# Kernel optimization log

Hardware: AMD Instinct MI355X
Metric: run time of the kernel (lower is better)

Reference implementation:

```python
import jax, jax.numpy as jnp
import numpy as np

THRESHOLD = 1.0
DECAY = 0.9


def setup_inputs() -> dict:
    key = jax.random.key(0)
    ks = jax.random.split(key, 5)
    B, T, I, H, O = 64, 256, 2048, 4096, 1024
    return {
        "x": jax.random.normal(ks[0], (B, T, I), dtype=jnp.float32),
        "W_in": jax.random.normal(ks[1], (I, H), dtype=jnp.float32) * (1.0 / np.sqrt(I)),
        "b_in": jax.random.normal(ks[2], (H,), dtype=jnp.float32) * 0.01,
        "W_out": jax.random.normal(ks[3], (H, O), dtype=jnp.float32) * (1.0 / np.sqrt(H)),
        "b_out": jax.random.normal(ks[4], (O,), dtype=jnp.float32) * 0.01,
        "m0": jnp.zeros((H,), dtype=jnp.float32),
    }


def reference(x, W_in, b_in, W_out, b_out, m0):
    # Batched input projection for all timesteps at once, then batch-mean
    # current per step: currents[t] = mean_b(Linear(x[:, t, :])).
    currents = jnp.einsum("bti,ih->th", x, W_in) / x.shape[0] + b_in  # [T, H]

    def step(m, c):
        m = DECAY * m + c                      # leaky integrate
        fired = m > THRESHOLD                  # threshold
        spike = fired.astype(m.dtype)
        m = jnp.where(fired, 0.0, m)           # reset fired neurons
        return m, spike

    _, spikes = jax.lax.scan(step, m0, currents)  # spikes: [T, H]
    agg = spikes.mean(axis=0)                     # [H]
    return agg @ W_out + b_out                    # [O]
```

## Files before the change

### kernel.cpp

```cpp
#include <hip/hip_runtime.h>

constexpr int B = 64, T = 256, I = 2048, H = 4096, O = 1024;

#define DECAY 0.9f
#define THRESH 1.0f

__global__ __launch_bounds__(256) void batch_reduce(const float* __restrict__ x,
                                                    float* __restrict__ xbar) {
    const int idx = blockIdx.x * 256 + threadIdx.x;
    const float4* x4 = (const float4*)x;
    const int stride4 = (T * I) / 4;
    float4 acc = {0.f, 0.f, 0.f, 0.f};
#pragma unroll 16
    for (int b = 0; b < B; ++b) {
        float4 v = x4[idx + b * stride4];
        acc.x += v.x; acc.y += v.y; acc.z += v.z; acc.w += v.w;
    }
    const float s = 1.0f / (float)B;
    acc.x *= s; acc.y *= s; acc.z *= s; acc.w *= s;
    ((float4*)xbar)[idx] = acc;
}

__global__ __launch_bounds__(256) void cur_init(const float* __restrict__ b_in,
                                                float* __restrict__ cur) {
    const int idx = blockIdx.x * 256 + threadIdx.x;
    const int h4 = idx & (H / 4 - 1);
    ((float4*)cur)[idx] = ((const float4*)b_in)[h4];
}

#define BM 64
#define BN 64
#define BK 16
#define KSPLIT 4
#define LDS_PAD 4

__global__ __launch_bounds__(256) void gemm_in(const float* __restrict__ A,
                                               const float* __restrict__ Bw,
                                               float* __restrict__ C) {
    __shared__ float As[BK][BM + LDS_PAD];
    __shared__ float Bs[BK][BN + LDS_PAD];

    const int tid = threadIdx.x;
    const int blockRow = blockIdx.y * BM;
    const int blockCol = blockIdx.x * BN;
    const int kBeg = blockIdx.z * (I / KSPLIT);
    const int kEnd = kBeg + (I / KSPLIT);

    const int tr = tid >> 4;
    const int tc = tid & 15;

    const int aRow = tid >> 2;
    const int aCol = (tid & 3) << 2;
    const int bRow = tid >> 4;
    const int bCol = (tid & 15) << 2;

    float acc[4][4];
#pragma unroll
    for (int i = 0; i < 4; ++i)
#pragma unroll
        for (int j = 0; j < 4; ++j) acc[i][j] = 0.f;

    for (int k0 = kBeg; k0 < kEnd; k0 += BK) {
        float4 av = *(const float4*)(&A[(blockRow + aRow) * I + k0 + aCol]);
        float4 bv = *(const float4*)(&Bw[(size_t)(k0 + bRow) * H + blockCol + bCol]);
        __syncthreads();
        As[aCol + 0][aRow] = av.x;
        As[aCol + 1][aRow] = av.y;
        As[aCol + 2][aRow] = av.z;
        As[aCol + 3][aRow] = av.w;
        *(float4*)(&Bs[bRow][bCol]) = bv;
        __syncthreads();

#pragma unroll
        for (int k = 0; k < BK; ++k) {
            float4 a = *(const float4*)(&As[k][tr << 2]);
            float4 b = *(const float4*)(&Bs[k][tc << 2]);
            const float ar[4] = {a.x, a.y, a.z, a.w};
            const float br[4] = {b.x, b.y, b.z, b.w};
#pragma unroll
            for (int i = 0; i < 4; ++i)
#pragma unroll
                for (int j = 0; j < 4; ++j) acc[i][j] += ar[i] * br[j];
        }
    }

#pragma unroll
    for (int i = 0; i < 4; ++i) {
        const int row = blockRow + (tr << 2) + i;
#pragma unroll
        for (int j = 0; j < 4; ++j) {
            atomicAdd(&C[(size_t)row * H + blockCol + (tc << 2) + j], acc[i][j]);
        }
    }
}

__global__ __launch_bounds__(256) void lif_scan(const float* __restrict__ cur,
                                                const float* __restrict__ m0,
                                                float* __restrict__ agg) {
    const int h = blockIdx.x * 256 + threadIdx.x;
    float m = m0[h];
    float count = 0.f;
    for (int t = 0; t < T; t += 16) {
        float c[16];
#pragma unroll
        for (int j = 0; j < 16; ++j) c[j] = cur[(size_t)(t + j) * H + h];
#pragma unroll
        for (int j = 0; j < 16; ++j) {
            m = DECAY * m + c[j];
            if (m > THRESH) { count += 1.f; m = 0.f; }
        }
    }
    agg[h] = count * (1.0f / (float)T);
}

__global__ __launch_bounds__(256) void out_init(const float* __restrict__ b_out,
                                                float* __restrict__ out) {
    const int o = blockIdx.x * 256 + threadIdx.x;
    out[o] = b_out[o];
}

__global__ __launch_bounds__(256) void out_gemv(const float* __restrict__ agg,
                                                const float* __restrict__ Wout,
                                                float* __restrict__ out) {
    const int o = blockIdx.x * 256 + threadIdx.x;
    const int h0 = blockIdx.y * 128;
    float s = 0.f;
#pragma unroll 8
    for (int h = h0; h < h0 + 128; ++h) {
        s += agg[h] * Wout[(size_t)h * O + o];
    }
    atomicAdd(&out[o], s);
}

extern "C" void kernel_launch(void* const* d_in, const int* in_sizes, int n_in,
                              void* d_out, int out_size, void* d_ws, size_t ws_size,
                              hipStream_t stream) {
    const float* x     = (const float*)d_in[0];
    const float* W_in  = (const float*)d_in[1];
    const float* b_in  = (const float*)d_in[2];
    const float* W_out = (const float*)d_in[3];
    const float* b_out = (const float*)d_in[4];
    const float* m0    = (const float*)d_in[5];
    float* out = (float*)d_out;

    float* xbar     = (float*)d_ws;
    float* currents = xbar + (size_t)T * I;
    float* agg      = currents + (size_t)T * H;

    batch_reduce<<<(T * I / 4) / 256, 256, 0, stream>>>(x, xbar);

    cur_init<<<(T * H / 4) / 256, 256, 0, stream>>>(b_in, currents);

    dim3 g2(H / BN, T / BM, KSPLIT);
    gemm_in<<<g2, 256, 0, stream>>>(xbar, W_in, currents);

    lif_scan<<<H / 256, 256, 0, stream>>>(currents, m0, agg);

    out_init<<<O / 256, 256, 0, stream>>>(b_out, out);
    dim3 g4(O / 256, H / 128);
    out_gemv<<<g4, 256, 0, stream>>>(agg, W_out, out);
}
```

Before: 331.7 us.

## Use split-bf16 MFMA for input GEMM and fuse split-K reduction into scan

The fp32 FMA tiled GEMM is replaced by a bf16x3 emulation (hi/lo splits) on MFMA 16x16x32 instructions. The batch-reduced input is stored pre-split as bf16 hi/lo, and W_in is split while being staged into LDS. When the workspace is large enough, split-K partials go to separate buffers and are summed with the bias inside the LIF scan, which drops the atomics and the init kernel. The scan block size and the output GEMV split are also changed. Accuracy is close to fp32 but not identical, which could flip threshold decisions.

Result: slower. 369.1 us (+11.3%).

```diff
diff --git a/kernel.cpp b/kernel.cpp
--- a/kernel.cpp
+++ b/kernel.cpp
@@ -5,8 +5,19 @@
 #define DECAY 0.9f
 #define THRESH 1.0f
 
+typedef __attribute__((ext_vector_type(8))) __bf16 bf16x8;
+typedef __attribute__((ext_vector_type(4))) float f32x4;
+
+__device__ inline void split_bf16(float a, unsigned short& hi, unsigned short& lo) {
+    unsigned int u = __float_as_uint(a);
+    hi = (unsigned short)(u >> 16);
+    float fhi = __uint_as_float(u & 0xffff0000u);
+    lo = (unsigned short)(__float_as_uint(a - fhi) >> 16);
+}
+
 __global__ __launch_bounds__(256) void batch_reduce(const float* __restrict__ x,
-                                                    float* __restrict__ xbar) {
+                                                    unsigned short* __restrict__ xh,
+                                                    unsigned short* __restrict__ xl) {
     const int idx = blockIdx.x * 256 + threadIdx.x;
     const float4* x4 = (const float4*)x;
     const int stride4 = (T * I) / 4;
@@ -17,8 +28,17 @@
         acc.x += v.x; acc.y += v.y; acc.z += v.z; acc.w += v.w;
     }
     const float s = 1.0f / (float)B;
-    acc.x *= s; acc.y *= s; acc.z *= s; acc.w *= s;
-    ((float4*)xbar)[idx] = acc;
+    float a[4] = {acc.x * s, acc.y * s, acc.z * s, acc.w * s};
+    unsigned short hi[4], lo[4];
+#pragma unroll
+    for (int j = 0; j < 4; ++j) split_bf16(a[j], hi[j], lo[j]);
+    uint2 ph, pl;
+    ph.x = (unsigned int)hi[0] | ((unsigned int)hi[1] << 16);
+    ph.y = (unsigned int)hi[2] | ((unsigned int)hi[3] << 16);
+    pl.x = (unsigned int)lo[0] | ((unsigned int)lo[1] << 16);
+    pl.y = (unsigned int)lo[2] | ((unsigned int)lo[3] << 16);
+    ((uint2*)xh)[idx] = ph;
+    ((uint2*)xl)[idx] = pl;
 }
 
 __global__ __launch_bounds__(256) void cur_init(const float* __restrict__ b_in,
@@ -28,89 +48,117 @@
     ((float4*)cur)[idx] = ((const float4*)b_in)[h4];
 }
 
-#define BM 64
-#define BN 64
-#define BK 16
+#define BN 32
+#define BK 32
 #define KSPLIT 4
-#define LDS_PAD 4
-
-__global__ __launch_bounds__(256) void gemm_in(const float* __restrict__ A,
-                                               const float* __restrict__ Bw,
-                                               float* __restrict__ C) {
-    __shared__ float As[BK][BM + LDS_PAD];
-    __shared__ float Bs[BK][BN + LDS_PAD];
+#define KCHUNK (I / KSPLIT)
+
+__global__ __launch_bounds__(256) void gemm_in(const unsigned short* __restrict__ xh,
+                                               const unsigned short* __restrict__ xl,
+                                               const float* __restrict__ Wi,
+                                               float* __restrict__ dst,
+                                               int useAtomic) {
+    __shared__ unsigned short BtH[BN][BK + 8];
+    __shared__ unsigned short BtL[BN][BK + 8];
 
     const int tid = threadIdx.x;
-    const int blockRow = blockIdx.y * BM;
-    const int blockCol = blockIdx.x * BN;
-    const int kBeg = blockIdx.z * (I / KSPLIT);
-    const int kEnd = kBeg + (I / KSPLIT);
-
-    const int tr = tid >> 4;
-    const int tc = tid & 15;
-
-    const int aRow = tid >> 2;
-    const int aCol = (tid & 3) << 2;
-    const int bRow = tid >> 4;
-    const int bCol = (tid & 15) << 2;
-
-    float acc[4][4];
-#pragma unroll
-    for (int i = 0; i < 4; ++i)
-#pragma unroll
-        for (int j = 0; j < 4; ++j) acc[i][j] = 0.f;
-
-    for (int k0 = kBeg; k0 < kEnd; k0 += BK) {
-        float4 av = *(const float4*)(&A[(blockRow + aRow) * I + k0 + aCol]);
-        float4 bv = *(const float4*)(&Bw[(size_t)(k0 + bRow) * H + blockCol + bCol]);
+    const int n0 = blockIdx.x * BN;
+    const int split = blockIdx.y;
+    const int kBeg = split * KCHUNK;
+    const int wave = tid >> 6, lane = tid & 63;
+    const int quad = lane >> 4, l16 = lane & 15;
+    const int m0 = wave * 64;
+
+    const int sn = tid & 31;
+    const int sk = (tid >> 5) << 2;
+
+    f32x4 acc[4][2];
+#pragma unroll
+    for (int mi = 0; mi < 4; ++mi)
+#pragma unroll
+        for (int ni = 0; ni < 2; ++ni) acc[mi][ni] = (f32x4){0.f, 0.f, 0.f, 0.f};
+
+    for (int k0 = kBeg; k0 < kBeg + KCHUNK; k0 += BK) {
+        const float* src = &Wi[(size_t)(k0 + sk) * H + n0 + sn];
+        float v0 = src[0], v1 = src[(size_t)H], v2 = src[(size_t)2 * H], v3 = src[(size_t)3 * H];
+
+        bf16x8 aH[4], aL[4];
+#pragma unroll
+        for (int mi = 0; mi < 4; ++mi) {
+            const size_t arow = (size_t)(m0 + mi * 16 + l16) * I + k0 + quad * 8;
+            aH[mi] = *(const bf16x8*)(xh + arow);
+            aL[mi] = *(const bf16x8*)(xl + arow);
+        }
+
+        unsigned short h0, h1, h2, h3, l0, l1, l2, l3;
+        split_bf16(v0, h0, l0); split_bf16(v1, h1, l1);
+        split_bf16(v2, h2, l2); split_bf16(v3, h3, l3);
+
         __syncthreads();
-        As[aCol + 0][aRow] = av.x;
-        As[aCol + 1][aRow] = av.y;
-        As[aCol + 2][aRow] = av.z;
-        As[aCol + 3][aRow] = av.w;
-        *(float4*)(&Bs[bRow][bCol]) = bv;
+        uint2 ph, pl;
+        ph.x = (unsigned int)h0 | ((unsigned int)h1 << 16);
+        ph.y = (unsigned int)h2 | ((unsigned int)h3 << 16);
+        pl.x = (unsigned int)l0 | ((unsigned int)l1 << 16);
+        pl.y = (unsigned int)l2 | ((unsigned int)l3 << 16);
+        *(uint2*)&BtH[sn][sk] = ph;
+        *(uint2*)&BtL[sn][sk] = pl;
         __syncthreads();
 
-#pragma unroll
-        for (int k = 0; k < BK; ++k) {
-            float4 a = *(const float4*)(&As[k][tr << 2]);
-            float4 b = *(const float4*)(&Bs[k][tc << 2]);
-            const float ar[4] = {a.x, a.y, a.z, a.w};
-            const float br[4] = {b.x, b.y, b.z, b.w};
-#pragma unroll
-            for (int i = 0; i < 4; ++i)
-#pragma unroll
-                for (int j = 0; j < 4; ++j) acc[i][j] += ar[i] * br[j];
-        }
-    }
-
-#pragma unroll
-    for (int i = 0; i < 4; ++i) {
-        const int row = blockRow + (tr << 2) + i;
-#pragma unroll
-        for (int j = 0; j < 4; ++j) {
-            atomicAdd(&C[(size_t)row * H + blockCol + (tc << 2) + j], acc[i][j]);
-        }
-    }
-}
-
-__global__ __launch_bounds__(256) void lif_scan(const float* __restrict__ cur,
-                                                const float* __restrict__ m0,
-                                                float* __restrict__ agg) {
-    const int h = blockIdx.x * 256 + threadIdx.x;
-    float m = m0[h];
-    float count = 0.f;
-    for (int t = 0; t < T; t += 16) {
-        float c[16];
-#pragma unroll
-        for (int j = 0; j < 16; ++j) c[j] = cur[(size_t)(t + j) * H + h];
-#pragma unroll
-        for (int j = 0; j < 16; ++j) {
+        bf16x8 bH[2], bL[2];
+#pragma unroll
+        for (int ni = 0; ni < 2; ++ni) {
+            bH[ni] = *(const bf16x8*)&BtH[ni * 16 + l16][quad * 8];
+            bL[ni] = *(const bf16x8*)&BtL[ni * 16 + l16][quad * 8];
+        }
+#pragma unroll
+        for (int mi = 0; mi < 4; ++mi)
+#pragma unroll
+            for (int ni = 0; ni < 2; ++ni) {
+                acc[mi][ni] = __builtin_amdgcn_mfma_f32_16x16x32_bf16(aL[mi], bH[ni], acc[mi][ni], 0, 0, 0);
+                acc[mi][ni] = __builtin_amdgcn_mfma_f32_16x16x32_bf16(aH[mi], bL[ni], acc[mi][ni], 0, 0, 0);
+                acc[mi][ni] = __builtin_amdgcn_mfma_f32_16x16x32_bf16(aH[mi], bH[ni], acc[mi][ni], 0, 0, 0);
+            }
+    }
+
+    float* base = useAtomic ? dst : dst + (size_t)split * T * H;
+#pragma unroll
+    for (int mi = 0; mi < 4; ++mi)
+#pragma unroll
+        for (int ni = 0; ni < 2; ++ni) {
+            const int h = n0 + ni * 16 + l16;
+#pragma unroll
+            for (int r = 0; r < 4; ++r) {
+                const int m = m0 + mi * 16 + quad * 4 + r;
+                if (useAtomic) atomicAdd(&base[(size_t)m * H + h], acc[mi][ni][r]);
+                else           base[(size_t)m * H + h] = acc[mi][ni][r];
+            }
+        }
+}
+
+__global__ __launch_bounds__(64) void lif_scan(const float* __restrict__ part,
+                                               const float* __restrict__ b_in,
+                                               const float* __restrict__ m0v,
+                                               float* __restrict__ agg,
+                                               int nsplit, int addBias) {
+    const int h = blockIdx.x * 64 + threadIdx.x;
+    const float bias = addBias ? b_in[h] : 0.f;
+    float m = m0v[h];
+    float cnt = 0.f;
+    for (int t0 = 0; t0 < T; t0 += 8) {
+        float c[8];
+#pragma unroll
+        for (int j = 0; j < 8; ++j) c[j] = bias;
+        for (int s = 0; s < nsplit; ++s) {
+#pragma unroll
+            for (int j = 0; j < 8; ++j) c[j] += part[((size_t)s * T + t0 + j) * H + h];
+        }
+#pragma unroll
+        for (int j = 0; j < 8; ++j) {
             m = DECAY * m + c[j];
-            if (m > THRESH) { count += 1.f; m = 0.f; }
-        }
-    }
-    agg[h] = count * (1.0f / (float)T);
+            if (m > THRESH) { cnt += 1.f; m = 0.f; }
+        }
+    }
+    agg[h] = cnt * (1.0f / (float)T);
 }
 
 __global__ __launch_bounds__(256) void out_init(const float* __restrict__ b_out,
@@ -123,11 +171,11 @@
                                                 const float* __restrict__ Wout,
                                                 float* __restrict__ out) {
     const int o = blockIdx.x * 256 + threadIdx.x;
-    const int h0 = blockIdx.y * 128;
+    const int h0 = blockIdx.y * 64;
     float s = 0.f;
 #pragma unroll 8
-    for (int h = h0; h < h0 + 128; ++h) {
-        s += agg[h] * Wout[(size_t)h * O + o];
+    for (int hh = h0; hh < h0 + 64; ++hh) {
+        s += agg[hh] * Wout[(size_t)hh * O + o];
     }
     atomicAdd(&out[o], s);
 }
@@ -143,20 +191,27 @@
     const float* m0    = (const float*)d_in[5];
     float* out = (float*)d_out;
 
-    float* xbar     = (float*)d_ws;
-    float* currents = xbar + (size_t)T * I;
-    float* agg      = currents + (size_t)T * H;
-
-    batch_reduce<<<(T * I / 4) / 256, 256, 0, stream>>>(x, xbar);
-
-    cur_init<<<(T * H / 4) / 256, 256, 0, stream>>>(b_in, currents);
-
-    dim3 g2(H / BN, T / BM, KSPLIT);
-    gemm_in<<<g2, 256, 0, stream>>>(xbar, W_in, currents);
-
-    lif_scan<<<H / 256, 256, 0, stream>>>(currents, m0, agg);
+    unsigned short* xh = (unsigned short*)d_ws;
+    unsigned short* xl = xh + (size_t)T * I;
+    float* agg  = (float*)(xl + (size_t)T * I);
+    float* part = agg + H;
+
+    const size_t need = (size_t)2 * T * I * 2 + (size_t)H * 4 + (size_t)KSPLIT * T * H * 4;
+    const int fits = (ws_size >= need) ? 1 : 0;
+
+    batch_reduce<<<(T * I / 4) / 256, 256, 0, stream>>>(x, xh, xl);
+
+    dim3 g2(H / BN, KSPLIT);
+    if (fits) {
+        gemm_in<<<g2, 256, 0, stream>>>(xh, xl, W_in, part, 0);
+        lif_scan<<<H / 64, 64, 0, stream>>>(part, b_in, m0, agg, KSPLIT, 1);
+    } else {
+        cur_init<<<(T * H / 4) / 256, 256, 0, stream>>>(b_in, part);
+        gemm_in<<<g2, 256, 0, stream>>>(xh, xl, W_in, part, 1);
+        lif_scan<<<H / 64, 64, 0, stream>>>(part, b_in, m0, agg, 1, 0);
+    }
 
     out_init<<<O / 256, 256, 0, stream>>>(b_out, out);
-    dim3 g4(O / 256, H / 128);
+    dim3 g4(O / 256, H / 64);
     out_gemv<<<g4, 256, 0, stream>>>(agg, W_out, out);
 }
```
